# Performance work log

Hardware: AMD Instinct MI355X
Metric: run time of the kernel (lower is better)

The kernel has to match this reference:

```python
import jax, jax.numpy as jnp
import numpy as np
from jax import lax

B, T, E = 64, 1024, 512
H, NSTACK = 512, 2


def setup_inputs() -> dict:
    key = jax.random.key(0)
    ks = jax.random.split(key, 7)
    seq = jax.random.normal(ks[0], (B, T, E), dtype=jnp.float32)
    seq_len = jax.random.randint(ks[1], (B,), 1, T + 1)
    seq_len = seq_len.at[0].set(T)  # torch sizes output by max(seq_len); pin it to T
    s = 1.0 / np.sqrt(H)
    W_ih = jax.random.uniform(ks[2], (NSTACK, 4 * H, E), jnp.float32, -s, s)
    W_hh = jax.random.uniform(ks[3], (NSTACK, 4 * H, H), jnp.float32, -s, s)
    b_ih = jax.random.uniform(ks[4], (NSTACK, 4 * H), jnp.float32, -s, s)
    b_hh = jax.random.uniform(ks[5], (NSTACK, 4 * H), jnp.float32, -s, s)
    return {"seq": seq, "seq_len": seq_len, "W_ih": W_ih, "W_hh": W_hh,
            "b_ih": b_ih, "b_hh": b_hh}


def _encoder_step(x, h, c, W_ih, W_hh, b_ih, b_hh):
    """One time step of the nStack residual LSTM. x:[B,E], h/c:[nStack,B,H]."""
    nh, nc = [], []
    inp = x
    for s in range(W_ih.shape[0]):
        gates = inp @ W_ih[s].T + h[s] @ W_hh[s].T + b_ih[s] + b_hh[s]
        i, f, g, o = jnp.split(gates, 4, axis=-1)
        i, f, o = jax.nn.sigmoid(i), jax.nn.sigmoid(f), jax.nn.sigmoid(o)
        g = jnp.tanh(g)
        cs = f * c[s] + i * g
        hs = o * jnp.tanh(cs)
        inp = hs + inp  # residual (E == H)
        nh.append(hs)
        nc.append(cs)
    return inp, jnp.stack(nh), jnp.stack(nc)


def reference(seq, seq_len, W_ih, W_hh, b_ih, b_hh):
    # Masked full-batch recurrence == torch's sorted shrinking-batch loop:
    # inactive rows (t >= seq_len) keep their state and write 0 hiddens.
    b, t, _ = seq.shape
    nstack = W_ih.shape[0]
    hidden = W_hh.shape[-1]
    h0 = jnp.zeros((nstack, b, hidden), seq.dtype)
    c0 = jnp.zeros((nstack, b, hidden), seq.dtype)
    mask_t = jnp.arange(t)[:, None] < seq_len[None, :]  # [T,B]

    def step(carry, xt):
        h, c = carry
        x, m = xt  # x:[B,E], m:[B]
        hx, nh, nc = _encoder_step(x, h, c, W_ih, W_hh, b_ih, b_hh)
        mm = m[None, :, None]
        h = jnp.where(mm, nh, h)
        c = jnp.where(mm, nc, c)
        out = jnp.where(m[:, None], hx, jnp.zeros_like(hx))
        return (h, c), out

    (h, c), outs = lax.scan(step, (h0, c0), (jnp.swapaxes(seq, 0, 1), mask_t))
    total_hiddens = jnp.swapaxes(outs, 0, 1)  # [B,T,H]
    return total_hiddens, h, c
```

## Files before the change

kernel.cpp:

```cpp
#include <hip/hip_runtime.h>
#include <stdint.h>

#define BB 64
#define TT 1024
#define HH 512
typedef unsigned long long ull;
typedef float v4f __attribute__((ext_vector_type(4)));
typedef short v8s __attribute__((ext_vector_type(8)));
typedef unsigned v4u __attribute__((ext_vector_type(4)));

__device__ __forceinline__ short f2bf(float f) {
    unsigned u = __float_as_uint(f);
    u += 0x7fffu + ((u >> 16) & 1u);
    return (short)(u >> 16);
}
__device__ __forceinline__ float sigmoidf_(float x) {
    x = fminf(fmaxf(x, -30.f), 30.f);
    return 1.f / (1.f + __expf(-x));
}
__device__ __forceinline__ float tanhf_(float x) {
    x = fminf(fmaxf(x, -15.f), 15.f);
    float e = __expf(2.f * x);
    return (e - 1.f) / (e + 1.f);
}

__device__ __forceinline__ unsigned aload32(const unsigned* p) {
    return __hip_atomic_load(p, __ATOMIC_RELAXED, __HIP_MEMORY_SCOPE_AGENT);
}
__device__ __forceinline__ void wait_ge(unsigned* c, unsigned tgt) {
    while (__hip_atomic_load(c, __ATOMIC_RELAXED, __HIP_MEMORY_SCOPE_AGENT) < tgt)
        __builtin_amdgcn_s_sleep(1);
}
__device__ __forceinline__ void stcc(unsigned* p, unsigned v) {
    asm volatile("global_store_dword %0, %1, off sc0 sc1" :: "v"(p), "v"(v) : "memory");
}
__device__ __forceinline__ void ld4cc(const unsigned* p, v4u& r0, v4u& r1, v4u& r2, v4u& r3) {
    asm volatile(
        "global_load_dwordx4 %0, %4, off sc0 sc1\n\t"
        "global_load_dwordx4 %1, %4, off offset:16 sc0 sc1\n\t"
        "global_load_dwordx4 %2, %4, off offset:2048 sc0 sc1\n\t"
        "global_load_dwordx4 %3, %4, off offset:2064 sc0 sc1\n\t"
        "s_waitcnt vmcnt(0)"
        : "=&v"(r0), "=&v"(r1), "=&v"(r2), "=&v"(r3)
        : "v"(p) : "memory");
}
__device__ __forceinline__ void ld8cc(const unsigned* px, const unsigned* ph,
        v4u& x0, v4u& x1, v4u& x2, v4u& x3, v4u& h0, v4u& h1, v4u& h2, v4u& h3) {
    asm volatile(
        "global_load_dwordx4 %0, %8, off sc0 sc1\n\t"
        "global_load_dwordx4 %1, %8, off offset:16 sc0 sc1\n\t"
        "global_load_dwordx4 %2, %8, off offset:2048 sc0 sc1\n\t"
        "global_load_dwordx4 %3, %8, off offset:2064 sc0 sc1\n\t"
        "global_load_dwordx4 %4, %9, off sc0 sc1\n\t"
        "global_load_dwordx4 %5, %9, off offset:16 sc0 sc1\n\t"
        "global_load_dwordx4 %6, %9, off offset:2048 sc0 sc1\n\t"
        "global_load_dwordx4 %7, %9, off offset:2064 sc0 sc1\n\t"
        "s_waitcnt vmcnt(0)"
        : "=&v"(x0), "=&v"(x1), "=&v"(x2), "=&v"(x3),
          "=&v"(h0), "=&v"(h1), "=&v"(h2), "=&v"(h3)
        : "v"(px), "v"(ph) : "memory");
}
__device__ __forceinline__ unsigned tagdiff(v4u a, v4u b, unsigned tg) {
    return ((a.x ^ tg) | (a.y ^ tg) | (a.z ^ tg) | (a.w ^ tg) |
            (b.x ^ tg) | (b.y ^ tg) | (b.z ^ tg) | (b.w ^ tg)) & 0xFFFFu;
}
__device__ __forceinline__ void packlds(short* dst, v4u a, v4u b) {
    v4u d;
    d.x = (a.x >> 16) | (a.y & 0xFFFF0000u);
    d.y = (a.z >> 16) | (a.w & 0xFFFF0000u);
    d.z = (b.x >> 16) | (b.y & 0xFFFF0000u);
    d.w = (b.z >> 16) | (b.w & 0xFFFF0000u);
    *(v4u*)dst = d;
}

__global__ __launch_bounds__(512, 1) void lstm_persistent_kernel(
    const float* __restrict__ seq, const int* __restrict__ seq_len,
    const float* __restrict__ W_ih, const float* __restrict__ W_hh,
    const float* __restrict__ b_ih, const float* __restrict__ b_hh,
    float* __restrict__ out, char* __restrict__ ws)
{
    __shared__ __align__(16) short act_lds[2048 * 8];
    __shared__ float gates_lds[4][16][32];

    const int gid = blockIdx.x;
    const int g   = gid & 3;
    const int s   = (gid >> 2) & 1;
    const int u0  = (gid >> 3) << 5;
    const int bg  = g << 4;
    const int tid = threadIdx.x;
    const int w   = tid >> 6;
    const int l   = tid & 63;
    const int q   = w >> 1;
    const int uh  = w & 1;
    const int quad = l >> 4, l15 = l & 15;
    const int cb  = tid >> 5, cu = tid & 31;

    unsigned* rc1 = (unsigned*)(ws + g * 256);
    unsigned* h0b = (unsigned*)(ws + 1024);
    unsigned* h1b = h0b + 4 * 4 * 16 * 512;
    unsigned* ibb = h1b + 4 * 4 * 16 * 512;

    const float* Wi = W_ih + (size_t)s * (2048 * 512);
    const float* Wh = W_hh + (size_t)s * (2048 * 512);
    const int row = q * 512 + u0 + uh * 16 + l15;
    v8s wf[32];
#pragma unroll
    for (int kt = 0; kt < 32; ++kt) {
        int ko = kt * 32 + quad * 8;
        const float* p = (ko < 512) ? (Wi + (size_t)row * 512 + ko)
                                    : (Wh + (size_t)row * 512 + (ko - 512));
        float4 x0 = *(const float4*)p;
        float4 x1 = *(const float4*)(p + 4);
        v8s v;
        v[0]=f2bf(x0.x); v[1]=f2bf(x0.y); v[2]=f2bf(x0.z); v[3]=f2bf(x0.w);
        v[4]=f2bf(x1.x); v[5]=f2bf(x1.y); v[6]=f2bf(x1.z); v[7]=f2bf(x1.w);
        wf[kt] = v;
    }
    float bias[4];
#pragma unroll
    for (int qq = 0; qq < 4; ++qq)
        bias[qq] = b_ih[s * 2048 + qq * 512 + u0 + cu] + b_hh[s * 2048 + qq * 512 + u0 + cu];
    const int len = seq_len[bg + cb];
    float hreg = 0.f, creg = 0.f;

    const int ch0 = 1024 + (tid << 1);
    const int mh  = ch0 & 15;
    const int kh  = (((ch0 >> 6) << 5) + (((ch0 >> 4) & 3) << 3)) - 512;
    const int cx0 = tid << 1;
    const int mx  = cx0 & 15;
    const int kx  = ((cx0 >> 6) << 5) + (((cx0 >> 4) & 3) << 3);
    unsigned* myhb = (s == 0) ? h0b : h1b;

    for (int tau = 0; tau <= TT; ++tau) {
        if (s == 0 && tau >= TT) break;
        if (s == 1 && tau == 0) continue;
        const int t   = (s == 0) ? tau : tau - 1;
        const int rb  = (((tau - 1) & 3) << 2 | g) << 13;
        const int wb  = ((tau & 3) << 2 | g) << 13;
        const unsigned tg = (unsigned)(tau - 1);
        float xres = 0.f;
        unsigned rcv = 0xFFFFFFFFu;

        if (s == 0) {
            if (tid == 0 && tau >= 4) rcv = aload32(rc1);
#pragma unroll
            for (int j = 0; j < 2; ++j) {
                int c = (j << 9) + tid;
                int ll = c & 63, m = ll & 15;
                int ko = ((c >> 6) << 5) + ((ll >> 4) << 3);
                const float* p = seq + (((size_t)(bg + m) * TT + t) << 9) + ko;
                float4 x0 = *(const float4*)p, x1 = *(const float4*)(p + 4);
                v8s v;
                v[0]=f2bf(x0.x); v[1]=f2bf(x0.y); v[2]=f2bf(x0.z); v[3]=f2bf(x0.w);
                v[4]=f2bf(x1.x); v[5]=f2bf(x1.y); v[6]=f2bf(x1.z); v[7]=f2bf(x1.w);
                *(v8s*)(act_lds + (size_t)c * 8) = v;
            }
            xres = seq[(((size_t)(bg + cb) * TT + t) << 9) + u0 + cu];
            if (tau == 0) {
                v4u zz = {0, 0, 0, 0};
                *(v4u*)(act_lds + (size_t)ch0 * 8) = zz;
                *(v4u*)(act_lds + (size_t)(ch0 + 1) * 8) = zz;
            } else {
                const unsigned* hp = h0b + rb + (mh << 9) + kh;
                for (;;) {
                    v4u r0, r1, r2, r3;
                    ld4cc(hp, r0, r1, r2, r3);
                    if ((tagdiff(r0, r1, tg) | tagdiff(r2, r3, tg)) == 0) {
                        packlds(act_lds + (size_t)ch0 * 8, r0, r1);
                        packlds(act_lds + (size_t)(ch0 + 1) * 8, r2, r3);
                        break;
                    }
                }
            }
        } else {
            const unsigned* px = ibb + rb + (mx << 9) + kx;
            if (tau == 1) {
                v4u zz = {0, 0, 0, 0};
                *(v4u*)(act_lds + (size_t)ch0 * 8) = zz;
                *(v4u*)(act_lds + (size_t)(ch0 + 1) * 8) = zz;
                for (;;) {
                    v4u r0, r1, r2, r3;
                    ld4cc(px, r0, r1, r2, r3);
                    if ((tagdiff(r0, r1, tg) | tagdiff(r2, r3, tg)) == 0) {
                        packlds(act_lds + (size_t)cx0 * 8, r0, r1);
                        packlds(act_lds + (size_t)(cx0 + 1) * 8, r2, r3);
                        break;
                    }
                }
            } else {
                const unsigned* ph = h1b + rb + (mh << 9) + kh;
                for (;;) {
                    v4u x0, x1, x2, x3, h0, h1, h2, h3;
                    ld8cc(px, ph, x0, x1, x2, x3, h0, h1, h2, h3);
                    if ((tagdiff(x0, x1, tg) | tagdiff(x2, x3, tg) |
                         tagdiff(h0, h1, tg) | tagdiff(h2, h3, tg)) == 0) {
                        packlds(act_lds + (size_t)cx0 * 8, x0, x1);
                        packlds(act_lds + (size_t)(cx0 + 1) * 8, x2, x3);
                        packlds(act_lds + (size_t)ch0 * 8, h0, h1);
                        packlds(act_lds + (size_t)(ch0 + 1) * 8, h2, h3);
                        break;
                    }
                }
            }
        }
        __syncthreads();
        if (s == 1 && tid == 0)
            __hip_atomic_fetch_add(rc1, 1u, __ATOMIC_RELAXED, __HIP_MEMORY_SCOPE_AGENT);

        v4f z = {0.f, 0.f, 0.f, 0.f};
        v4f acc0 = z, acc1 = z, acc2 = z, acc3 = z;
#pragma unroll
        for (int kt = 0; kt < 32; kt += 4) {
            v8s a0 = *(const v8s*)(act_lds + ((kt + 0) * 64 + l) * 8);
            v8s a1 = *(const v8s*)(act_lds + ((kt + 1) * 64 + l) * 8);
            v8s a2 = *(const v8s*)(act_lds + ((kt + 2) * 64 + l) * 8);
            v8s a3 = *(const v8s*)(act_lds + ((kt + 3) * 64 + l) * 8);
            acc0 = __builtin_amdgcn_mfma_f32_16x16x32_bf16(a0, wf[kt + 0], acc0, 0, 0, 0);
            acc1 = __builtin_amdgcn_mfma_f32_16x16x32_bf16(a1, wf[kt + 1], acc1, 0, 0, 0);
            acc2 = __builtin_amdgcn_mfma_f32_16x16x32_bf16(a2, wf[kt + 2], acc2, 0, 0, 0);
            acc3 = __builtin_amdgcn_mfma_f32_16x16x32_bf16(a3, wf[kt + 3], acc3, 0, 0, 0);
        }
        v4f af = (acc0 + acc1) + (acc2 + acc3);
#pragma unroll
        for (int r = 0; r < 4; ++r)
            gates_lds[q][quad * 4 + r][uh * 16 + l15] = af[r];
        __syncthreads();

        float gi = gates_lds[0][cb][cu] + bias[0];
        float gf = gates_lds[1][cb][cu] + bias[1];
        float gg = gates_lds[2][cb][cu] + bias[2];
        float go = gates_lds[3][cb][cu] + bias[3];
        float ii = sigmoidf_(gi), ff = sigmoidf_(gf);
        float gv = tanhf_(gg),   oo = sigmoidf_(go);
        float cs = ff * creg + ii * gv;
        float hs = oo * tanhf_(cs);
        const bool msk = (t < len);
        if (msk) { creg = cs; hreg = hs; }
        float i1s = 0.f;
        if (s == 0) {
            i1s = hs + xres;
        } else {
            int k  = u0 + cu;
            int cI = ((k >> 5) << 6) + (((k >> 3) & 3) << 4) + cb;
            unsigned short us = (unsigned short)act_lds[cI * 8 + (k & 7)];
            float i1 = __uint_as_float(((unsigned)us) << 16);
            out[(((size_t)(bg + cb) * TT + t) << 9) + u0 + cu] = msk ? (i1 + hs) : 0.f;
        }
        if (s == 0 && tid == 0 && tau >= 4) {
            unsigned need = 16u * (unsigned)(tau - 3);
            if (rcv < need) wait_ge(rc1, need);
        }
        __syncthreads();

        const unsigned otg = (unsigned)tau;
        const int widx = wb + (cb << 9) + u0 + cu;
        if (s == 0) {
            stcc(h0b + widx, (((unsigned)(unsigned short)f2bf(hreg)) << 16) | otg);
            stcc(ibb + widx, (((unsigned)(unsigned short)f2bf(i1s)) << 16) | otg);
        } else {
            stcc(h1b + widx, (((unsigned)(unsigned short)f2bf(hreg)) << 16) | otg);
        }
    }

    const size_t OH = (size_t)BB * TT * HH;
    const size_t hoff = OH + (size_t)s * BB * HH + ((size_t)(bg + cb) << 9) + u0 + cu;
    out[hoff] = hreg;
    out[hoff + (size_t)2 * BB * HH] = creg;
}

extern "C" void kernel_launch(void* const* d_in, const int* in_sizes, int n_in,
                              void* d_out, int out_size, void* d_ws, size_t ws_size,
                              hipStream_t stream) {
    const float* seq     = (const float*)d_in[0];
    const int*   seq_len = (const int*)d_in[1];
    const float* W_ih    = (const float*)d_in[2];
    const float* W_hh    = (const float*)d_in[3];
    const float* b_ih    = (const float*)d_in[4];
    const float* b_hh    = (const float*)d_in[5];
    float* out = (float*)d_out;

    hipMemsetAsync(d_ws, 0, 1024, stream);

    lstm_persistent_kernel<<<dim3(128), dim3(512), 0, stream>>>(
        seq, seq_len, W_ih, W_hh, b_ih, b_hh, out, (char*)d_ws);
}
```

Before: 4.098 ms.

## Prefetch layer-0 hidden state early and drop end-of-step barrier in recurrent loop

Layer 0 now issues its tagged load of the previous hidden state before the input staging and only waits on it afterwards, so load latency overlaps the seq conversion. Layer 1 polls its input and hidden buffers independently and accepts each as soon as its tag matches, instead of reloading both. The i1 value is read from LDS before the MFMA loop, and the third __syncthreads per step is removed. The ring-buffer credit wait is now done by every thread just before its own ibb store rather than by thread 0 before a barrier. This shortens the per-step critical path of the sequential recurrence, but removing the barrier relies on per-thread credit waits and the LDS reuse ordering still being correct, and it adds more atomic polling traffic.

```diff
diff --git a/kernel.cpp b/kernel.cpp
--- a/kernel.cpp
+++ b/kernel.cpp
@@ -43,6 +43,19 @@
         "s_waitcnt vmcnt(0)"
         : "=&v"(r0), "=&v"(r1), "=&v"(r2), "=&v"(r3)
         : "v"(p) : "memory");
+}
+__device__ __forceinline__ void ld4cc_issue(const unsigned* p, v4u& r0, v4u& r1, v4u& r2, v4u& r3) {
+    asm volatile(
+        "global_load_dwordx4 %0, %4, off sc0 sc1\n\t"
+        "global_load_dwordx4 %1, %4, off offset:16 sc0 sc1\n\t"
+        "global_load_dwordx4 %2, %4, off offset:2048 sc0 sc1\n\t"
+        "global_load_dwordx4 %3, %4, off offset:2064 sc0 sc1"
+        : "=&v"(r0), "=&v"(r1), "=&v"(r2), "=&v"(r3)
+        : "v"(p) : "memory");
+}
+__device__ __forceinline__ void vmwait4(v4u& r0, v4u& r1, v4u& r2, v4u& r3) {
+    asm volatile("s_waitcnt vmcnt(0)"
+        : "+v"(r0), "+v"(r1), "+v"(r2), "+v"(r3) :: "memory");
 }
 __device__ __forceinline__ void ld8cc(const unsigned* px, const unsigned* ph,
         v4u& x0, v4u& x1, v4u& x2, v4u& x3, v4u& h0, v4u& h1, v4u& h2, v4u& h3) {
@@ -142,7 +155,10 @@
         unsigned rcv = 0xFFFFFFFFu;
 
         if (s == 0) {
-            if (tid == 0 && tau >= 4) rcv = aload32(rc1);
+            v4u p0, p1, p2, p3;
+            const unsigned* hp = h0b + rb + (mh << 9) + kh;
+            if (tau >= 1) ld4cc_issue(hp, p0, p1, p2, p3);
+            if (tau >= 4) rcv = aload32(rc1);
 #pragma unroll
             for (int j = 0; j < 2; ++j) {
                 int c = (j << 9) + tid;
@@ -161,14 +177,19 @@
                 *(v4u*)(act_lds + (size_t)ch0 * 8) = zz;
                 *(v4u*)(act_lds + (size_t)(ch0 + 1) * 8) = zz;
             } else {
-                const unsigned* hp = h0b + rb + (mh << 9) + kh;
-                for (;;) {
-                    v4u r0, r1, r2, r3;
-                    ld4cc(hp, r0, r1, r2, r3);
-                    if ((tagdiff(r0, r1, tg) | tagdiff(r2, r3, tg)) == 0) {
-                        packlds(act_lds + (size_t)ch0 * 8, r0, r1);
-                        packlds(act_lds + (size_t)(ch0 + 1) * 8, r2, r3);
-                        break;
+                vmwait4(p0, p1, p2, p3);
+                if ((tagdiff(p0, p1, tg) | tagdiff(p2, p3, tg)) == 0) {
+                    packlds(act_lds + (size_t)ch0 * 8, p0, p1);
+                    packlds(act_lds + (size_t)(ch0 + 1) * 8, p2, p3);
+                } else {
+                    for (;;) {
+                        v4u r0, r1, r2, r3;
+                        ld4cc(hp, r0, r1, r2, r3);
+                        if ((tagdiff(r0, r1, tg) | tagdiff(r2, r3, tg)) == 0) {
+                            packlds(act_lds + (size_t)ch0 * 8, r0, r1);
+                            packlds(act_lds + (size_t)(ch0 + 1) * 8, r2, r3);
+                            break;
+                        }
                     }
                 }
             }
@@ -189,16 +210,35 @@
                 }
             } else {
                 const unsigned* ph = h1b + rb + (mh << 9) + kh;
-                for (;;) {
-                    v4u x0, x1, x2, x3, h0, h1, h2, h3;
-                    ld8cc(px, ph, x0, x1, x2, x3, h0, h1, h2, h3);
-                    if ((tagdiff(x0, x1, tg) | tagdiff(x2, x3, tg) |
-                         tagdiff(h0, h1, tg) | tagdiff(h2, h3, tg)) == 0) {
+                v4u x0, x1, x2, x3, h0, h1, h2, h3;
+                ld8cc(px, ph, x0, x1, x2, x3, h0, h1, h2, h3);
+                int xok = (tagdiff(x0, x1, tg) | tagdiff(x2, x3, tg)) == 0;
+                int hok = (tagdiff(h0, h1, tg) | tagdiff(h2, h3, tg)) == 0;
+                if (xok) {
+                    packlds(act_lds + (size_t)cx0 * 8, x0, x1);
+                    packlds(act_lds + (size_t)(cx0 + 1) * 8, x2, x3);
+                }
+                if (hok) {
+                    packlds(act_lds + (size_t)ch0 * 8, h0, h1);
+                    packlds(act_lds + (size_t)(ch0 + 1) * 8, h2, h3);
+                }
+                while (!(xok & hok)) {
+                    if (!xok & !hok) {
+                        ld8cc(px, ph, x0, x1, x2, x3, h0, h1, h2, h3);
+                    } else if (!xok) {
+                        ld4cc(px, x0, x1, x2, x3);
+                    } else {
+                        ld4cc(ph, h0, h1, h2, h3);
+                    }
+                    if (!xok && (tagdiff(x0, x1, tg) | tagdiff(x2, x3, tg)) == 0) {
+                        xok = 1;
                         packlds(act_lds + (size_t)cx0 * 8, x0, x1);
                         packlds(act_lds + (size_t)(cx0 + 1) * 8, x2, x3);
+                    }
+                    if (!hok && (tagdiff(h0, h1, tg) | tagdiff(h2, h3, tg)) == 0) {
+                        hok = 1;
                         packlds(act_lds + (size_t)ch0 * 8, h0, h1);
                         packlds(act_lds + (size_t)(ch0 + 1) * 8, h2, h3);
-                        break;
                     }
                 }
             }
@@ -206,6 +246,13 @@
         __syncthreads();
         if (s == 1 && tid == 0)
             __hip_atomic_fetch_add(rc1, 1u, __ATOMIC_RELAXED, __HIP_MEMORY_SCOPE_AGENT);
+        float i1v = 0.f;
+        if (s == 1) {
+            int k  = u0 + cu;
+            int cI = ((k >> 5) << 6) + (((k >> 3) & 3) << 4) + cb;
+            unsigned short us = (unsigned short)act_lds[cI * 8 + (k & 7)];
+            i1v = __uint_as_float(((unsigned)us) << 16);
+        }
 
         v4f z = {0.f, 0.f, 0.f, 0.f};
         v4f acc0 = z, acc1 = z, acc2 = z, acc3 = z;
@@ -236,29 +283,19 @@
         float hs = oo * tanhf_(cs);
         const bool msk = (t < len);
         if (msk) { creg = cs; hreg = hs; }
-        float i1s = 0.f;
-        if (s == 0) {
-            i1s = hs + xres;
-        } else {
-            int k  = u0 + cu;
-            int cI = ((k >> 5) << 6) + (((k >> 3) & 3) << 4) + cb;
-            unsigned short us = (unsigned short)act_lds[cI * 8 + (k & 7)];
-            float i1 = __uint_as_float(((unsigned)us) << 16);
-            out[(((size_t)(bg + cb) * TT + t) << 9) + u0 + cu] = msk ? (i1 + hs) : 0.f;
-        }
-        if (s == 0 && tid == 0 && tau >= 4) {
-            unsigned need = 16u * (unsigned)(tau - 3);
-            if (rcv < need) wait_ge(rc1, need);
-        }
-        __syncthreads();
 
         const unsigned otg = (unsigned)tau;
         const int widx = wb + (cb << 9) + u0 + cu;
+        stcc(myhb + widx, (((unsigned)(unsigned short)f2bf(hreg)) << 16) | otg);
         if (s == 0) {
-            stcc(h0b + widx, (((unsigned)(unsigned short)f2bf(hreg)) << 16) | otg);
+            float i1s = hs + xres;
+            if (tau >= 4) {
+                unsigned need = 16u * (unsigned)(tau - 3);
+                if (rcv < need) wait_ge(rc1, need);
+            }
             stcc(ibb + widx, (((unsigned)(unsigned short)f2bf(i1s)) << 16) | otg);
         } else {
-            stcc(h1b + widx, (((unsigned)(unsigned short)f2bf(hreg)) << 16) | otg);
+            out[(((size_t)(bg + cb) * TT + t) << 9) + u0 + cu] = msk ? (i1v + hs) : 0.f;
         }
     }
 
```

After: 5.139 ms. +25.4%, slower.
